# Performance work log

Hardware: AMD Instinct MI355X
Metric: run time of the kernel (lower is better)

Reference implementation:

```python
import jax, jax.numpy as jnp
import numpy as np

N = 100000
E = 1600000
D = 128      # input feature dim
H = 128      # hidden_channels
O = 2        # out_channels
NEG_SLOPE = 0.2
EPS = 1e-16  # PyG softmax denominator epsilon


def gat_conv(x, src, dst, W_src, W_dst, att_src, att_dst, bias):
    """PyG GATConv, heads=1, add_self_loops=False, concat=True."""
    xs = x @ W_src                      # [N, C]
    xd = x @ W_dst                      # [N, C]
    a_s = xs @ att_src                  # [N]
    a_d = xd @ att_dst                  # [N]
    e = jax.nn.leaky_relu(a_s[src] + a_d[dst], NEG_SLOPE)   # [E]
    # segment softmax over edges grouped by destination node
    m = jax.ops.segment_max(e, dst, num_segments=N)          # [N]
    m = jnp.where(jnp.isfinite(m), m, 0.0)
    ex = jnp.exp(e - m[dst])                                  # [E]
    denom = jax.ops.segment_sum(ex, dst, num_segments=N)      # [N]
    alpha = ex / (denom[dst] + EPS)                            # [E]
    msg = alpha[:, None] * xs[src]                             # [E, C]
    out = jax.ops.segment_sum(msg, dst, num_segments=N)       # [N, C]
    return out + bias


def setup_inputs() -> dict:
    key = jax.random.key(0)
    ks = jax.random.split(key, 14)
    s = lambda k, shape, fan: jax.random.normal(k, shape, jnp.float32) * (1.0 / np.sqrt(fan))
    x = jax.random.normal(ks[0], (N, D), jnp.float32)
    edge_index = jax.random.randint(ks[1], (2, E), 0, N, dtype=jnp.int32)
    return {
        "x": x,
        "edge_index": edge_index,
        "W1s": s(ks[2], (D, H), D), "W1d": s(ks[3], (D, H), D),
        "a1s": s(ks[4], (H,), H),   "a1d": s(ks[5], (H,), H),
        "b1": jnp.zeros((H,), jnp.float32),
        "W2s": s(ks[6], (H, H), H), "W2d": s(ks[7], (H, H), H),
        "a2s": s(ks[8], (H,), H),   "a2d": s(ks[9], (H,), H),
        "b2": jnp.zeros((H,), jnp.float32),
        "Wl": s(ks[10], (H, O), H), "bl": jnp.zeros((O,), jnp.float32),
    }


def reference(x, edge_index, W1s, W1d, a1s, a1d, b1, W2s, W2d, a2s, a2d, b2, Wl, bl):
    src, dst = edge_index[0], edge_index[1]
    h = jax.nn.relu(gat_conv(x, src, dst, W1s, W1d, a1s, a1d, b1))
    # dropout p=0.3 is identity at inference
    h = jax.nn.relu(gat_conv(h, src, dst, W2s, W2d, a2s, a2d, b2))
    return h @ Wl + bl  # [N, O]
```

## Files before the change

kernel.cpp:

```cpp
#include <hip/hip_runtime.h>
#include <hip/hip_fp16.h>

#define NBSHIFT 8
#define BSZ     256
#define CAP     5120

typedef _Float16 f16x8 __attribute__((ext_vector_type(8)));
typedef float    f32x4 __attribute__((ext_vector_type(4)));


#define GEMM_LDS_BYTES (128 * 136 * 2 + 512)

template <bool XHALF>
__device__ __forceinline__ void gemm_body(
        const void* __restrict__ Xv, const float* __restrict__ Ws,
        const float* __restrict__ Wd, const float* __restrict__ attd,
        const float* __restrict__ att,
        __half* __restrict__ Y, float* __restrict__ a_s, float* __restrict__ a_d,
        int N, int blk, char* smem) {
    _Float16 (*sWh)[136] = (_Float16(*)[136])smem;
    float* svd = (float*)(smem + 128 * 136 * 2);
    int t = threadIdx.x;

    if (t < 128) {
        const float4* wr = (const float4*)&Wd[t * 128];
        const float4* ar = (const float4*)attd;
        float s = 0.f;
#pragma unroll 8
        for (int j = 0; j < 32; j++) {
            float4 w = wr[j], a = ar[j];
            s += w.x * a.x + w.y * a.y + w.z * a.z + w.w * a.w;
        }
        svd[t] = s;
    }
#pragma unroll
    for (int i = 0; i < 16; i++) {
        int gid = t + i * 256;
        int n = gid & 127, kq = gid >> 7;
        _Float16 p[4];
        p[0] = (_Float16)Ws[(kq * 4 + 0) * 128 + n];
        p[1] = (_Float16)Ws[(kq * 4 + 1) * 128 + n];
        p[2] = (_Float16)Ws[(kq * 4 + 2) * 128 + n];
        p[3] = (_Float16)Ws[(kq * 4 + 3) * 128 + n];
        *(uint2*)&sWh[n][kq * 4] = *(uint2*)p;
    }
    __syncthreads();

    int l = t & 63, wv = t >> 6;
    int quad = l >> 4, lm = l & 15;
    int rbase = blk * 64 + wv * 16;
    int arow = rbase + lm;
    bool rok = arow < N;

    f32x4 acc[8];
#pragma unroll
    for (int c = 0; c < 8; c++) acc[c] = (f32x4){0.f, 0.f, 0.f, 0.f};
    float adp = 0.f;

#pragma unroll
    for (int kc = 0; kc < 4; kc++) {
        int k0 = kc * 32 + quad * 8;
        float xf[8];
        f16x8 af;
        if constexpr (XHALF) {
            const __half* xrow = (const __half*)Xv + (size_t)arow * 128;
            if (rok) {
                af = *(const f16x8*)&xrow[k0];
            } else {
#pragma unroll
                for (int j = 0; j < 8; j++) af[j] = (_Float16)0.f;
            }
#pragma unroll
            for (int j = 0; j < 8; j++) xf[j] = (float)af[j];
        } else {
            const float* xrow = (const float*)Xv + (size_t)arow * 128;
            if (rok) {
                *(float4*)&xf[0] = *(const float4*)&xrow[k0];
                *(float4*)&xf[4] = *(const float4*)&xrow[k0 + 4];
            } else {
#pragma unroll
                for (int j = 0; j < 8; j++) xf[j] = 0.f;
            }
#pragma unroll
            for (int j = 0; j < 8; j++) af[j] = (_Float16)xf[j];
        }
        float4 v0 = *(const float4*)&svd[k0];
        float4 v1 = *(const float4*)&svd[k0 + 4];
        adp += xf[0] * v0.x + xf[1] * v0.y + xf[2] * v0.z + xf[3] * v0.w
             + xf[4] * v1.x + xf[5] * v1.y + xf[6] * v1.z + xf[7] * v1.w;
#pragma unroll
        for (int c = 0; c < 8; c++) {
            f16x8 bf = *(const f16x8*)&sWh[c * 16 + lm][k0];
            acc[c] = __builtin_amdgcn_mfma_f32_16x16x32_f16(af, bf, acc[c], 0, 0, 0);
        }
    }

    adp += __shfl_xor(adp, 16);
    adp += __shfl_xor(adp, 32);
    if (quad == 0 && rok) a_d[arow] = adp;

    float attc[8];
#pragma unroll
    for (int c = 0; c < 8; c++) attc[c] = att[c * 16 + lm];
#pragma unroll
    for (int r = 0; r < 4; r++) {
        int grow = rbase + quad * 4 + r;
        bool gok = grow < N;
        float p = 0.f;
#pragma unroll
        for (int c = 0; c < 8; c++) {
            if (gok) Y[(size_t)grow * 128 + c * 16 + lm] = __float2half(acc[c][r]);
            p += acc[c][r] * attc[c];
        }
        p += __shfl_xor(p, 1); p += __shfl_xor(p, 2); p += __shfl_xor(p, 4); p += __shfl_xor(p, 8);
        if (lm == 0 && gok) a_s[grow] = p;
    }
}

__global__ __launch_bounds__(256, 4) void k_fuse1(
        const float* __restrict__ X, const float* __restrict__ W1s,
        const float* __restrict__ W1d, const float* __restrict__ a1d,
        const float* __restrict__ a1s,
        __half* __restrict__ Y, float* __restrict__ a_s, float* __restrict__ a_d, int N, int gb,
        const int* __restrict__ src, const int* __restrict__ dst, int E,
        int* __restrict__ cursor, unsigned* __restrict__ pairs) {
    __shared__ __align__(16) char smem[GEMM_LDS_BYTES];
    int t = threadIdx.x;

    if ((int)blockIdx.x >= gb) {
        int* hist  = (int*)smem;
        int* start = hist + 512;
        hist[t] = 0; hist[t + 256] = 0;
        __syncthreads();
        int e0 = (blockIdx.x - gb) * 1024 + t * 4;
        int d[4], s[4];
        bool full = (e0 + 3 < E);
        if (full) {
            int4 dv = *(const int4*)&dst[e0];
            int4 sv = *(const int4*)&src[e0];
            d[0] = dv.x; d[1] = dv.y; d[2] = dv.z; d[3] = dv.w;
            s[0] = sv.x; s[1] = sv.y; s[2] = sv.z; s[3] = sv.w;
#pragma unroll
            for (int i = 0; i < 4; i++) atomicAdd(&hist[d[i] >> NBSHIFT], 1);
        } else {
#pragma unroll
            for (int i = 0; i < 4; i++) {
                if (e0 + i < E) { d[i] = dst[e0 + i]; s[i] = src[e0 + i]; atomicAdd(&hist[d[i] >> NBSHIFT], 1); }
                else d[i] = -1;
            }
        }
        __syncthreads();
        if (hist[t] > 0)       start[t]       = atomicAdd(&cursor[t],       hist[t]);
        if (hist[t + 256] > 0) start[t + 256] = atomicAdd(&cursor[t + 256], hist[t + 256]);
        __syncthreads();
        hist[t] = 0; hist[t + 256] = 0;
        __syncthreads();
#pragma unroll
        for (int i = 0; i < 4; i++) {
            if (full || (e0 + i < E)) {
                int b = d[i] >> NBSHIFT;
                int r = atomicAdd(&hist[b], 1);
                pairs[b * CAP + start[b] + r] = ((unsigned)(d[i] & (BSZ - 1)) << 17) | (unsigned)s[i];
            }
        }
        return;
    }

    gemm_body<false>(X, W1s, W1d, a1d, a1s, Y, a_s, a_d, N, blockIdx.x, smem);
}

__global__ __launch_bounds__(256, 4) void k_gemm2(
        const __half* __restrict__ X, const float* __restrict__ W2s,
        const float* __restrict__ W2d, const float* __restrict__ a2d,
        const float* __restrict__ a2s,
        __half* __restrict__ Y, float* __restrict__ a_s, float* __restrict__ a_d, int N) {
    __shared__ __align__(16) char smem[GEMM_LDS_BYTES];
    gemm_body<true>(X, W2s, W2d, a2d, a2s, Y, a_s, a_d, N, blockIdx.x, smem);
}

__global__ __launch_bounds__(256) void kB_csr(const unsigned* __restrict__ pairs,
                                              const int* __restrict__ cursor,
                                              int* __restrict__ row_start, int* __restrict__ row_end,
                                              int* __restrict__ csr_src, int N) {
    __shared__ int cnt[BSZ];
    __shared__ int cur[BSZ];
    __shared__ int sS[256];
    int b = blockIdx.x, t = threadIdx.x;
    int base = b * CAP;
    int ecnt = cursor[b];
    int nodeBase = b << NBSHIFT;
    cnt[t] = 0;
    __syncthreads();
    for (int j = t; j < ecnt; j += 256)
        atomicAdd(&cnt[pairs[base + j] >> 17], 1);
    __syncthreads();
    int c0 = cnt[t];
    sS[t] = c0; __syncthreads();
    for (int off = 1; off < 256; off <<= 1) {
        int x = (t >= off) ? sS[t - off] : 0;
        __syncthreads();
        sS[t] += x;
        __syncthreads();
    }
    int excl = sS[t] - c0;
    cur[t] = excl;
    int g = nodeBase + t;
    if (g < N) { row_start[g] = base + excl; row_end[g] = base + excl + c0; }
    __syncthreads();
    for (int j = t; j < ecnt; j += 256) {
        unsigned p = pairs[base + j];
        int r = atomicAdd(&cur[p >> 17], 1);
        csr_src[base + r] = (int)(p & 0x1FFFFu);
    }
}


__device__ __forceinline__ void fma_mix2(float& a0, float& a1, unsigned h2, float w) {
    asm("v_fma_mix_f32 %0, %1, %2, %0 op_sel_hi:[1,0,0]" : "+v"(a0) : "v"(h2), "v"(w));
    asm("v_fma_mix_f32 %0, %1, %2, %0 op_sel:[1,0,0] op_sel_hi:[1,0,0]" : "+v"(a1) : "v"(h2), "v"(w));
}

#define ACC_MIX(u, wj)  do {                                    \
    const unsigned* _w32 = (const unsigned*)&(u);               \
    fma_mix2(acc[0], acc[1], _w32[0], (wj));                    \
    fma_mix2(acc[2], acc[3], _w32[1], (wj));                    \
    fma_mix2(acc[4], acc[5], _w32[2], (wj));                    \
    fma_mix2(acc[6], acc[7], _w32[3], (wj));                    \
} while (0)

template <bool HEAD>
__global__ __launch_bounds__(256, 6) void k_agg(const int* __restrict__ csr_src, const int* __restrict__ row_start,
                                                const int* __restrict__ row_end,
                                                const float* __restrict__ a_s, const float* __restrict__ a_d,
                                                const __half* __restrict__ xs, const float* __restrict__ bias,
                                                const float* __restrict__ Wl, const float* __restrict__ bl,
                                                void* __restrict__ outv, int N) {
    __shared__ int2 sP[4][64];
    int t = threadIdx.x; int wv = t >> 6, l = t & 63;
    int n = blockIdx.x * 4 + wv;
    if (n >= N) return;
    int rs = row_start[n], re = row_end[n];
    int deg = re - rs;
    float adn = a_d[n];
    int q = l >> 4;
    int c = (l & 15) * 8;
    const int* cs = csr_src + rs;
    int2* sp = sP[wv];

    float acc[8];
#pragma unroll
    for (int k = 0; k < 8; k++) acc[k] = 0.f;
    float dnl = 0.f;

    for (int base = 0; base < deg; base += 64) {
        int m = deg - base; if (m > 64) m = 64;
        int idx = 0; float w = 0.f;
        if (l < m) {
            idx = cs[base + l];
            float tv = a_s[idx] + adn;
            tv = tv > 0.f ? tv : 0.2f * tv;
            w = __expf(tv);
        }
        dnl += w;
        sp[l] = make_int2(idx, __float_as_int(w));
        int mc = (m + 3) & ~3;
        int e = q;
        for (; e + 12 < mc; e += 16) {
            int2 p0 = sp[e];
            int2 p1 = sp[e + 4];
            int2 p2 = sp[e + 8];
            int2 p3 = sp[e + 12];
            uint4 u0 = *(const uint4*)&xs[(size_t)p0.x * 128 + c];
            uint4 u1 = *(const uint4*)&xs[(size_t)p1.x * 128 + c];
            uint4 u2 = *(const uint4*)&xs[(size_t)p2.x * 128 + c];
            uint4 u3 = *(const uint4*)&xs[(size_t)p3.x * 128 + c];
            ACC_MIX(u0, __int_as_float(p0.y));
            ACC_MIX(u1, __int_as_float(p1.y));
            ACC_MIX(u2, __int_as_float(p2.y));
            ACC_MIX(u3, __int_as_float(p3.y));
        }
        for (; e + 4 < mc; e += 8) {
            int2 p0 = sp[e];
            int2 p1 = sp[e + 4];
            uint4 u0 = *(const uint4*)&xs[(size_t)p0.x * 128 + c];
            uint4 u1 = *(const uint4*)&xs[(size_t)p1.x * 128 + c];
            ACC_MIX(u0, __int_as_float(p0.y));
            ACC_MIX(u1, __int_as_float(p1.y));
        }
        for (; e < mc; e += 4) {
            int2 p0 = sp[e];
            uint4 u0 = *(const uint4*)&xs[(size_t)p0.x * 128 + c];
            ACC_MIX(u0, __int_as_float(p0.y));
        }
    }

    dnl += __shfl_xor(dnl, 1);
    dnl += __shfl_xor(dnl, 2);
    dnl += __shfl_xor(dnl, 4);
    dnl += __shfl_xor(dnl, 8);
    dnl += __shfl_xor(dnl, 16);
    dnl += __shfl_xor(dnl, 32);
    float inv = 1.f / (dnl + 1e-16f);

    float hv[8];
    float4 b0 = *(const float4*)&bias[c];
    float4 b1 = *(const float4*)&bias[c + 4];
    float bb[8] = {b0.x, b0.y, b0.z, b0.w, b1.x, b1.y, b1.z, b1.w};
#pragma unroll
    for (int k = 0; k < 8; k++) {
        float v = acc[k];
        v += __shfl_xor(v, 16);
        v += __shfl_xor(v, 32);
        v = v * inv + bb[k];
        hv[k] = v > 0.f ? v : 0.f;
    }

    if (HEAD) {
        float p0 = 0.f, p1 = 0.f;
#pragma unroll
        for (int k = 0; k < 8; k++) {
            p0 += hv[k] * Wl[2 * (c + k)];
            p1 += hv[k] * Wl[2 * (c + k) + 1];
        }
#pragma unroll
        for (int o = 8; o > 0; o >>= 1) { p0 += __shfl_xor(p0, o); p1 += __shfl_xor(p1, o); }
        float* out = (float*)outv;
        if (l == 0) { out[2 * n] = p0 + bl[0]; out[2 * n + 1] = p1 + bl[1]; }
    } else {
        if (q == 0) {
            __half* hout = (__half*)outv;
            __half hb[8];
#pragma unroll
            for (int k = 0; k < 8; k++) hb[k] = __float2half(hv[k]);
            *(uint4*)&hout[(size_t)n * 128 + c] = *(uint4*)hb;
        }
    }
}


extern "C" void kernel_launch(void* const* d_in, const int* in_sizes, int n_in,
                              void* d_out, int out_size, void* d_ws, size_t ws_size,
                              hipStream_t stream) {
    const float* x   = (const float*)d_in[0];
    const int*   ei  = (const int*)d_in[1];
    const float* W1s = (const float*)d_in[2];
    const float* W1d = (const float*)d_in[3];
    const float* a1s = (const float*)d_in[4];
    const float* a1d = (const float*)d_in[5];
    const float* b1  = (const float*)d_in[6];
    const float* W2s = (const float*)d_in[7];
    const float* W2d = (const float*)d_in[8];
    const float* a2s = (const float*)d_in[9];
    const float* a2d = (const float*)d_in[10];
    const float* b2  = (const float*)d_in[11];
    const float* Wl  = (const float*)d_in[12];
    const float* bl  = (const float*)d_in[13];
    float* out = (float*)d_out;

    int N = in_sizes[0] / 128;
    int E = in_sizes[1] / 2;
    const int* srcA = ei;
    const int* dstA = ei + E;
    int NB = (N + BSZ - 1) >> NBSHIFT;

    __half* xs = (__half*)d_ws;
    __half* h  = xs + (size_t)N * 128;
    float* as_ = (float*)(h + (size_t)N * 128);
    float* ad_ = as_ + N;
    int* row_start = (int*)(ad_ + N);
    int* row_end   = row_start + N;
    int* csr_src   = row_end + N;
    int* cursor    = csr_src + (size_t)NB * CAP;
    unsigned* pairs = (unsigned*)h;

    int gb = (N + 63) / 64;
    int EB = (E + 1023) / 1024;
    int ab = (N + 3) / 4;

    hipMemsetAsync(cursor, 0, (size_t)NB * 4, stream);

    k_fuse1<<<gb + EB, 256, 0, stream>>>(x, W1s, W1d, a1d, a1s, xs, as_, ad_, N, gb,
                                         srcA, dstA, E, cursor, pairs);

    kB_csr<<<NB, 256, 0, stream>>>(pairs, cursor, row_start, row_end, csr_src, N);

    k_agg<false><<<ab, 256, 0, stream>>>(csr_src, row_start, row_end, as_, ad_, xs, b1, nullptr, nullptr, h, N);

    k_gemm2<<<gb, 256, 0, stream>>>(h, W2s, W2d, a2d, a2s, xs, as_, ad_, N);

    k_agg<true><<<ab, 256, 0, stream>>>(csr_src, row_start, row_end, as_, ad_, xs, b2, Wl, bl, out, N);
}
```

Measured before the change: 326.1 us.

## Slice features into channel-major blocks and precompute normalized edge weights

Stores xs and h in a sliced layout of [8][N][16] halves so that each aggregation block gathers only one 16-channel slice per source node. A new kernel, kW, precomputes the softmax-normalized edge weights into a (src, weight) array before aggregation. k_slice then handles four nodes per wave on one slice, aiming for better cache locality per slice. The head output is accumulated across slices with atomics into a pre-zeroed buffer. This adds an extra kernel and an extra pass over the edge array per layer, re-reads the edge list once per slice, and uses float atomics.

```diff
diff --git a/kernel.cpp b/kernel.cpp
--- a/kernel.cpp
+++ b/kernel.cpp
@@ -4,6 +4,7 @@
 #define NBSHIFT 8
 #define BSZ     256
 #define CAP     5120
+#define NSLICE  8
 
 typedef _Float16 f16x8 __attribute__((ext_vector_type(8)));
 typedef float    f32x4 __attribute__((ext_vector_type(4)));
@@ -63,9 +64,10 @@
         float xf[8];
         f16x8 af;
         if constexpr (XHALF) {
-            const __half* xrow = (const __half*)Xv + (size_t)arow * 128;
+            const __half* xp = (const __half*)Xv +
+                ((size_t)(k0 >> 4) * N + arow) * 16 + (k0 & 15);
             if (rok) {
-                af = *(const f16x8*)&xrow[k0];
+                af = *(const f16x8*)xp;
             } else {
 #pragma unroll
                 for (int j = 0; j < 8; j++) af[j] = (_Float16)0.f;
@@ -109,7 +111,7 @@
         float p = 0.f;
 #pragma unroll
         for (int c = 0; c < 8; c++) {
-            if (gok) Y[(size_t)grow * 128 + c * 16 + lm] = __float2half(acc[c][r]);
+            if (gok) Y[((size_t)c * N + grow) * 16 + lm] = __float2half(acc[c][r]);
             p += acc[c][r] * attc[c];
         }
         p += __shfl_xor(p, 1); p += __shfl_xor(p, 2); p += __shfl_xor(p, 4); p += __shfl_xor(p, 8);
@@ -214,125 +216,126 @@
     }
 }
 
+__global__ __launch_bounds__(256) void kW(const int* __restrict__ csr_src,
+                                          const int* __restrict__ rs_, const int* __restrict__ re_,
+                                          const float* __restrict__ a_s, const float* __restrict__ a_d,
+                                          int2* __restrict__ ew, int N) {
+    int t = threadIdx.x; int wv = t >> 6, l = t & 63;
+    int n = blockIdx.x * 4 + wv;
+    if (n >= N) return;
+    int rs = rs_[n];
+    int deg = re_[n] - rs;
+    float adn = a_d[n];
+
+    if (deg <= 64) {
+        int sidx = 0; float w = 0.f;
+        if (l < deg) {
+            sidx = csr_src[rs + l];
+            float tv = a_s[sidx] + adn;
+            tv = tv > 0.f ? tv : 0.2f * tv;
+            w = __expf(tv);
+        }
+        float dn = w;
+        dn += __shfl_xor(dn, 1);  dn += __shfl_xor(dn, 2);
+        dn += __shfl_xor(dn, 4);  dn += __shfl_xor(dn, 8);
+        dn += __shfl_xor(dn, 16); dn += __shfl_xor(dn, 32);
+        float inv = 1.f / (dn + 1e-16f);
+        if (l < deg) ew[rs + l] = make_int2(sidx, __float_as_int(w * inv));
+    } else {
+        float dn = 0.f;
+        for (int b = 0; b < deg; b += 64) {
+            if (b + l < deg) {
+                int s = csr_src[rs + b + l];
+                float tv = a_s[s] + adn;
+                tv = tv > 0.f ? tv : 0.2f * tv;
+                dn += __expf(tv);
+            }
+        }
+        dn += __shfl_xor(dn, 1);  dn += __shfl_xor(dn, 2);
+        dn += __shfl_xor(dn, 4);  dn += __shfl_xor(dn, 8);
+        dn += __shfl_xor(dn, 16); dn += __shfl_xor(dn, 32);
+        float inv = 1.f / (dn + 1e-16f);
+        for (int b = 0; b < deg; b += 64) {
+            if (b + l < deg) {
+                int s = csr_src[rs + b + l];
+                float tv = a_s[s] + adn;
+                tv = tv > 0.f ? tv : 0.2f * tv;
+                ew[rs + b + l] = make_int2(s, __float_as_int(__expf(tv) * inv));
+            }
+        }
+    }
+}
+
 
 __device__ __forceinline__ void fma_mix2(float& a0, float& a1, unsigned h2, float w) {
     asm("v_fma_mix_f32 %0, %1, %2, %0 op_sel_hi:[1,0,0]" : "+v"(a0) : "v"(h2), "v"(w));
     asm("v_fma_mix_f32 %0, %1, %2, %0 op_sel:[1,0,0] op_sel_hi:[1,0,0]" : "+v"(a1) : "v"(h2), "v"(w));
 }
 
-#define ACC_MIX(u, wj)  do {                                    \
-    const unsigned* _w32 = (const unsigned*)&(u);               \
-    fma_mix2(acc[0], acc[1], _w32[0], (wj));                    \
-    fma_mix2(acc[2], acc[3], _w32[1], (wj));                    \
-    fma_mix2(acc[4], acc[5], _w32[2], (wj));                    \
-    fma_mix2(acc[6], acc[7], _w32[3], (wj));                    \
-} while (0)
-
 template <bool HEAD>
-__global__ __launch_bounds__(256, 6) void k_agg(const int* __restrict__ csr_src, const int* __restrict__ row_start,
-                                                const int* __restrict__ row_end,
-                                                const float* __restrict__ a_s, const float* __restrict__ a_d,
-                                                const __half* __restrict__ xs, const float* __restrict__ bias,
-                                                const float* __restrict__ Wl, const float* __restrict__ bl,
-                                                void* __restrict__ outv, int N) {
-    __shared__ int2 sP[4][64];
+__global__ __launch_bounds__(256) void k_slice(const int2* __restrict__ ew,
+                                               const int* __restrict__ rs_, const int* __restrict__ re_,
+                                               const __half* __restrict__ xs,
+                                               const float* __restrict__ bias,
+                                               const float* __restrict__ Wl, const float* __restrict__ bl,
+                                               void* __restrict__ outv, int N) {
     int t = threadIdx.x; int wv = t >> 6, l = t & 63;
-    int n = blockIdx.x * 4 + wv;
-    if (n >= N) return;
-    int rs = row_start[n], re = row_end[n];
-    int deg = re - rs;
-    float adn = a_d[n];
-    int q = l >> 4;
-    int c = (l & 15) * 8;
-    const int* cs = csr_src + rs;
-    int2* sp = sP[wv];
-
-    float acc[8];
-#pragma unroll
-    for (int k = 0; k < 8; k++) acc[k] = 0.f;
-    float dnl = 0.f;
-
-    for (int base = 0; base < deg; base += 64) {
-        int m = deg - base; if (m > 64) m = 64;
-        int idx = 0; float w = 0.f;
-        if (l < m) {
-            idx = cs[base + l];
-            float tv = a_s[idx] + adn;
-            tv = tv > 0.f ? tv : 0.2f * tv;
-            w = __expf(tv);
-        }
-        dnl += w;
-        sp[l] = make_int2(idx, __float_as_int(w));
-        int mc = (m + 3) & ~3;
-        int e = q;
-        for (; e + 12 < mc; e += 16) {
-            int2 p0 = sp[e];
-            int2 p1 = sp[e + 4];
-            int2 p2 = sp[e + 8];
-            int2 p3 = sp[e + 12];
-            uint4 u0 = *(const uint4*)&xs[(size_t)p0.x * 128 + c];
-            uint4 u1 = *(const uint4*)&xs[(size_t)p1.x * 128 + c];
-            uint4 u2 = *(const uint4*)&xs[(size_t)p2.x * 128 + c];
-            uint4 u3 = *(const uint4*)&xs[(size_t)p3.x * 128 + c];
-            ACC_MIX(u0, __int_as_float(p0.y));
-            ACC_MIX(u1, __int_as_float(p1.y));
-            ACC_MIX(u2, __int_as_float(p2.y));
-            ACC_MIX(u3, __int_as_float(p3.y));
-        }
-        for (; e + 4 < mc; e += 8) {
-            int2 p0 = sp[e];
-            int2 p1 = sp[e + 4];
-            uint4 u0 = *(const uint4*)&xs[(size_t)p0.x * 128 + c];
-            uint4 u1 = *(const uint4*)&xs[(size_t)p1.x * 128 + c];
-            ACC_MIX(u0, __int_as_float(p0.y));
-            ACC_MIX(u1, __int_as_float(p1.y));
-        }
-        for (; e < mc; e += 4) {
-            int2 p0 = sp[e];
-            uint4 u0 = *(const uint4*)&xs[(size_t)p0.x * 128 + c];
-            ACC_MIX(u0, __int_as_float(p0.y));
-        }
-    }
-
-    dnl += __shfl_xor(dnl, 1);
-    dnl += __shfl_xor(dnl, 2);
-    dnl += __shfl_xor(dnl, 4);
-    dnl += __shfl_xor(dnl, 8);
-    dnl += __shfl_xor(dnl, 16);
-    dnl += __shfl_xor(dnl, 32);
-    float inv = 1.f / (dnl + 1e-16f);
-
-    float hv[8];
-    float4 b0 = *(const float4*)&bias[c];
-    float4 b1 = *(const float4*)&bias[c + 4];
-    float bb[8] = {b0.x, b0.y, b0.z, b0.w, b1.x, b1.y, b1.z, b1.w};
-#pragma unroll
-    for (int k = 0; k < 8; k++) {
-        float v = acc[k];
-        v += __shfl_xor(v, 16);
-        v += __shfl_xor(v, 32);
-        v = v * inv + bb[k];
-        hv[k] = v > 0.f ? v : 0.f;
-    }
+    int slice = blockIdx.x & (NSLICE - 1);
+    int g = blockIdx.x >> 3;
+    if (g * 16 + wv * 4 >= N) return;
+    int q   = l >> 4;
+    int ql  = l & 15;
+    int qe  = ql >> 2;
+    int sub = ql & 3;
+    int n = g * 16 + wv * 4 + q;
+    bool nok = n < N;
+    int rs = 0, deg = 0;
+    if (nok) { rs = rs_[n]; deg = re_[n] - rs; }
+    const __half* xb = xs + (size_t)slice * N * 16;
+
+    float a0 = 0.f, a1 = 0.f, a2 = 0.f, a3 = 0.f;
+    for (int b = 0; b < deg; b += 4) {
+        int i = b + qe;
+        long long pv = 0;
+        if (i < deg) pv = __builtin_nontemporal_load((const long long*)(ew + rs + i));
+        int   sidx = (int)(unsigned)(pv & 0xffffffffll);
+        float w    = __int_as_float((int)(pv >> 32));
+        uint2 u = *(const uint2*)&xb[(size_t)sidx * 16 + sub * 4];
+        fma_mix2(a0, a1, u.x, w);
+        fma_mix2(a2, a3, u.y, w);
+    }
+    a0 += __shfl_xor(a0, 4); a0 += __shfl_xor(a0, 8);
+    a1 += __shfl_xor(a1, 4); a1 += __shfl_xor(a1, 8);
+    a2 += __shfl_xor(a2, 4); a2 += __shfl_xor(a2, 8);
+    a3 += __shfl_xor(a3, 4); a3 += __shfl_xor(a3, 8);
+
+    int ch = slice * 16 + sub * 4;
+    float4 bv = *(const float4*)&bias[ch];
+    float h0 = a0 + bv.x; h0 = h0 > 0.f ? h0 : 0.f;
+    float h1 = a1 + bv.y; h1 = h1 > 0.f ? h1 : 0.f;
+    float h2 = a2 + bv.z; h2 = h2 > 0.f ? h2 : 0.f;
+    float h3 = a3 + bv.w; h3 = h3 > 0.f ? h3 : 0.f;
 
     if (HEAD) {
-        float p0 = 0.f, p1 = 0.f;
-#pragma unroll
-        for (int k = 0; k < 8; k++) {
-            p0 += hv[k] * Wl[2 * (c + k)];
-            p1 += hv[k] * Wl[2 * (c + k) + 1];
-        }
-#pragma unroll
-        for (int o = 8; o > 0; o >>= 1) { p0 += __shfl_xor(p0, o); p1 += __shfl_xor(p1, o); }
-        float* out = (float*)outv;
-        if (l == 0) { out[2 * n] = p0 + bl[0]; out[2 * n + 1] = p1 + bl[1]; }
+        float4 wA = *(const float4*)&Wl[2 * ch];
+        float4 wB = *(const float4*)&Wl[2 * ch + 4];
+        float p0 = h0 * wA.x + h1 * wA.z + h2 * wB.x + h3 * wB.z;
+        float p1 = h0 * wA.y + h1 * wA.w + h2 * wB.y + h3 * wB.w;
+        p0 += __shfl_xor(p0, 1); p0 += __shfl_xor(p0, 2);
+        p1 += __shfl_xor(p1, 1); p1 += __shfl_xor(p1, 2);
+        if (ql == 0 && nok) {
+            if (slice == 0) { p0 += bl[0]; p1 += bl[1]; }
+            float* out = (float*)outv;
+            atomicAdd(&out[2 * n],     p0);
+            atomicAdd(&out[2 * n + 1], p1);
+        }
     } else {
-        if (q == 0) {
+        if (qe == 0 && nok) {
+            __half hh[4];
+            hh[0] = __float2half(h0); hh[1] = __float2half(h1);
+            hh[2] = __float2half(h2); hh[3] = __float2half(h3);
             __half* hout = (__half*)outv;
-            __half hb[8];
-#pragma unroll
-            for (int k = 0; k < 8; k++) hb[k] = __float2half(hv[k]);
-            *(uint4*)&hout[(size_t)n * 128 + c] = *(uint4*)hb;
+            *(uint2*)&hout[((size_t)slice * N + n) * 16 + sub * 4] = *(uint2*)hh;
         }
     }
 }
@@ -371,22 +374,29 @@
     int* row_end   = row_start + N;
     int* csr_src   = row_end + N;
     int* cursor    = csr_src + (size_t)NB * CAP;
+    int2* ew = (int2*)(((uintptr_t)(cursor + NB) + 15) & ~(uintptr_t)15);
     unsigned* pairs = (unsigned*)h;
 
     int gb = (N + 63) / 64;
     int EB = (E + 1023) / 1024;
-    int ab = (N + 3) / 4;
+    int wb = (N + 3) / 4;
+    int sgrid = NSLICE * ((N + 15) / 16);
 
     hipMemsetAsync(cursor, 0, (size_t)NB * 4, stream);
+    hipMemsetAsync(out, 0, (size_t)N * 2 * sizeof(float), stream);
 
     k_fuse1<<<gb + EB, 256, 0, stream>>>(x, W1s, W1d, a1d, a1s, xs, as_, ad_, N, gb,
                                          srcA, dstA, E, cursor, pairs);
 
     kB_csr<<<NB, 256, 0, stream>>>(pairs, cursor, row_start, row_end, csr_src, N);
 
-    k_agg<false><<<ab, 256, 0, stream>>>(csr_src, row_start, row_end, as_, ad_, xs, b1, nullptr, nullptr, h, N);
+    kW<<<wb, 256, 0, stream>>>(csr_src, row_start, row_end, as_, ad_, ew, N);
+
+    k_slice<false><<<sgrid, 256, 0, stream>>>(ew, row_start, row_end, xs, b1, nullptr, nullptr, h, N);
 
     k_gemm2<<<gb, 256, 0, stream>>>(h, W2s, W2d, a2d, a2s, xs, as_, ad_, N);
 
-    k_agg<true><<<ab, 256, 0, stream>>>(csr_src, row_start, row_end, as_, ad_, xs, b2, Wl, bl, out, N);
-}
+    kW<<<wb, 256, 0, stream>>>(csr_src, row_start, row_end, as_, ad_, ew, N);
+
+    k_slice<true><<<sgrid, 256, 0, stream>>>(ew, row_start, row_end, xs, b2, Wl, bl, out, N);
+}
```

Measured after the change: 609.3 us. +86.9%, slower.

## Map one destination node per 16-lane group in aggregation kernel

Applied to the files above, without the earlier changes.

The aggregation kernel now processes 4 destination nodes per wavefront (one per 16-lane quarter) instead of one node per wavefront split across 4 edge subsets. Each quarter walks its own node's edges in 16-edge rounds, which removes the cross-quarter shuffle reductions of the accumulators and denominator and avoids idle lanes for low-degree nodes (average degree is about 16). The cost is divergence: every quarter loops for the wavefront's maximum round count, and high-degree nodes are no longer spread across the whole wavefront.

```diff
diff --git a/kernel.cpp b/kernel.cpp
--- a/kernel.cpp
+++ b/kernel.cpp
@@ -229,68 +229,59 @@
 } while (0)
 
 template <bool HEAD>
-__global__ __launch_bounds__(256, 6) void k_agg(const int* __restrict__ csr_src, const int* __restrict__ row_start,
-                                                const int* __restrict__ row_end,
+__global__ __launch_bounds__(256, 6) void k_agg(const int* __restrict__ csr_src, const int* __restrict__ rs_,
+                                                const int* __restrict__ re_,
                                                 const float* __restrict__ a_s, const float* __restrict__ a_d,
                                                 const __half* __restrict__ xs, const float* __restrict__ bias,
                                                 const float* __restrict__ Wl, const float* __restrict__ bl,
                                                 void* __restrict__ outv, int N) {
-    __shared__ int2 sP[4][64];
+    __shared__ int2 sP[4][4][16];
     int t = threadIdx.x; int wv = t >> 6, l = t & 63;
-    int n = blockIdx.x * 4 + wv;
-    if (n >= N) return;
-    int rs = row_start[n], re = row_end[n];
-    int deg = re - rs;
-    float adn = a_d[n];
-    int q = l >> 4;
-    int c = (l & 15) * 8;
-    const int* cs = csr_src + rs;
-    int2* sp = sP[wv];
+    int q = l >> 4, es = l & 15;
+    int n = blockIdx.x * 16 + wv * 4 + q;
+    bool nok = n < N;
+    int rs0 = 0, deg = 0;
+    if (nok) { rs0 = rs_[n]; deg = re_[n] - rs0; }
+    float adn = nok ? a_d[n] : 0.f;
+    const int* cs = csr_src + rs0;
+    int c = es * 8;
+
+    int R = (deg + 15) >> 4;
+    R = max(R, __shfl_xor(R, 16));
+    R = max(R, __shfl_xor(R, 32));
 
     float acc[8];
 #pragma unroll
     for (int k = 0; k < 8; k++) acc[k] = 0.f;
     float dnl = 0.f;
-
-    for (int base = 0; base < deg; base += 64) {
-        int m = deg - base; if (m > 64) m = 64;
+    int2 (*sq)[16] = sP[wv];
+
+    for (int r = 0; r < R; ++r) {
+        int i = r * 16 + es;
         int idx = 0; float w = 0.f;
-        if (l < m) {
-            idx = cs[base + l];
+        if (i < deg) {
+            idx = cs[i];
             float tv = a_s[idx] + adn;
             tv = tv > 0.f ? tv : 0.2f * tv;
             w = __expf(tv);
         }
         dnl += w;
-        sp[l] = make_int2(idx, __float_as_int(w));
-        int mc = (m + 3) & ~3;
-        int e = q;
-        for (; e + 12 < mc; e += 16) {
-            int2 p0 = sp[e];
-            int2 p1 = sp[e + 4];
-            int2 p2 = sp[e + 8];
-            int2 p3 = sp[e + 12];
-            uint4 u0 = *(const uint4*)&xs[(size_t)p0.x * 128 + c];
-            uint4 u1 = *(const uint4*)&xs[(size_t)p1.x * 128 + c];
-            uint4 u2 = *(const uint4*)&xs[(size_t)p2.x * 128 + c];
-            uint4 u3 = *(const uint4*)&xs[(size_t)p3.x * 128 + c];
-            ACC_MIX(u0, __int_as_float(p0.y));
-            ACC_MIX(u1, __int_as_float(p1.y));
-            ACC_MIX(u2, __int_as_float(p2.y));
-            ACC_MIX(u3, __int_as_float(p3.y));
-        }
-        for (; e + 4 < mc; e += 8) {
-            int2 p0 = sp[e];
-            int2 p1 = sp[e + 4];
-            uint4 u0 = *(const uint4*)&xs[(size_t)p0.x * 128 + c];
-            uint4 u1 = *(const uint4*)&xs[(size_t)p1.x * 128 + c];
-            ACC_MIX(u0, __int_as_float(p0.y));
-            ACC_MIX(u1, __int_as_float(p1.y));
-        }
-        for (; e < mc; e += 4) {
-            int2 p0 = sp[e];
-            uint4 u0 = *(const uint4*)&xs[(size_t)p0.x * 128 + c];
-            ACC_MIX(u0, __int_as_float(p0.y));
+        sq[q][es] = make_int2(idx, __float_as_int(w));
+
+        int rem = deg - r * 16;
+        int mcq = rem >= 16 ? 16 : (rem > 0 ? ((rem + 3) & ~3) : 0);
+        const int2* spq = sq[q];
+        for (int e = 0; e < mcq; e += 4) {
+            int4 pA = *(const int4*)&spq[e];
+            int4 pB = *(const int4*)&spq[e + 2];
+            uint4 u0 = *(const uint4*)&xs[(size_t)pA.x * 128 + c];
+            uint4 u1 = *(const uint4*)&xs[(size_t)pA.z * 128 + c];
+            uint4 u2 = *(const uint4*)&xs[(size_t)pB.x * 128 + c];
+            uint4 u3 = *(const uint4*)&xs[(size_t)pB.z * 128 + c];
+            ACC_MIX(u0, __int_as_float(pA.y));
+            ACC_MIX(u1, __int_as_float(pA.w));
+            ACC_MIX(u2, __int_as_float(pB.y));
+            ACC_MIX(u3, __int_as_float(pB.w));
         }
     }
 
@@ -298,8 +289,6 @@
     dnl += __shfl_xor(dnl, 2);
     dnl += __shfl_xor(dnl, 4);
     dnl += __shfl_xor(dnl, 8);
-    dnl += __shfl_xor(dnl, 16);
-    dnl += __shfl_xor(dnl, 32);
     float inv = 1.f / (dnl + 1e-16f);
 
     float hv[8];
@@ -308,10 +297,7 @@
     float bb[8] = {b0.x, b0.y, b0.z, b0.w, b1.x, b1.y, b1.z, b1.w};
 #pragma unroll
     for (int k = 0; k < 8; k++) {
-        float v = acc[k];
-        v += __shfl_xor(v, 16);
-        v += __shfl_xor(v, 32);
-        v = v * inv + bb[k];
+        float v = acc[k] * inv + bb[k];
         hv[k] = v > 0.f ? v : 0.f;
     }
 
@@ -322,12 +308,17 @@
             p0 += hv[k] * Wl[2 * (c + k)];
             p1 += hv[k] * Wl[2 * (c + k) + 1];
         }
-#pragma unroll
-        for (int o = 8; o > 0; o >>= 1) { p0 += __shfl_xor(p0, o); p1 += __shfl_xor(p1, o); }
-        float* out = (float*)outv;
-        if (l == 0) { out[2 * n] = p0 + bl[0]; out[2 * n + 1] = p1 + bl[1]; }
+        p0 += __shfl_xor(p0, 1); p0 += __shfl_xor(p0, 2);
+        p0 += __shfl_xor(p0, 4); p0 += __shfl_xor(p0, 8);
+        p1 += __shfl_xor(p1, 1); p1 += __shfl_xor(p1, 2);
+        p1 += __shfl_xor(p1, 4); p1 += __shfl_xor(p1, 8);
+        if (es == 0 && nok) {
+            float* out = (float*)outv;
+            out[2 * n]     = p0 + bl[0];
+            out[2 * n + 1] = p1 + bl[1];
+        }
     } else {
-        if (q == 0) {
+        if (nok) {
             __half* hout = (__half*)outv;
             __half hb[8];
 #pragma unroll
@@ -375,7 +366,7 @@
 
     int gb = (N + 63) / 64;
     int EB = (E + 1023) / 1024;
-    int ab = (N + 3) / 4;
+    int ab = (N + 15) / 16;
 
     hipMemsetAsync(cursor, 0, (size_t)NB * 4, stream);
 
```

New measurement: 319.7 us. Within noise of the previous version (-2.0%).
